# Kernel optimization log

Hardware: AMD Instinct MI355X
Metric: run time of the kernel (lower is better)

## Reference

```python
import jax, jax.numpy as jnp
import numpy as np

B, S, D, H = 2, 2048, 1024, 16
DK = D // H


def setup_inputs() -> dict:
    key = jax.random.key(0)
    ks = jax.random.split(key, 11)
    s = 1.0 / np.sqrt(D)
    return {
        "q": jax.random.normal(ks[0], (B, S, D), jnp.float32),
        "k": jax.random.normal(ks[1], (B, S, D), jnp.float32),
        "v": jax.random.normal(ks[2], (B, S, D), jnp.float32),
        "mask": jnp.ones((B, 1, S, S), jnp.int32),
        "Wq": jax.random.normal(ks[3], (D, D), jnp.float32) * s,
        "bq": jnp.zeros((D,), jnp.float32),
        "Wk": jax.random.normal(ks[4], (D, D), jnp.float32) * s,
        "bk": jnp.zeros((D,), jnp.float32),
        "Wv": jax.random.normal(ks[5], (D, D), jnp.float32) * s,
        "bv": jnp.zeros((D,), jnp.float32),
        "Wo": jax.random.normal(ks[6], (D, D), jnp.float32) * s,
        "bo": jnp.zeros((D,), jnp.float32),
    }


def reference(q, k, v, mask, Wq, bq, Wk, bk, Wv, bv, Wo, bo):
    # Note: original torch code calls non-in-place masked_fill and discards the
    # result, so the mask has no mathematical effect; we preserve that.
    qh = (q @ Wq + bq).reshape(B, S, H, DK).transpose(0, 2, 1, 3)  # [B,H,S,DK]
    kh = (k @ Wk + bk).reshape(B, S, H, DK).transpose(0, 2, 1, 3)
    vh = (v @ Wv + bv).reshape(B, S, H, DK).transpose(0, 2, 1, 3)
    scores = jnp.einsum("bhqd,bhkd->bhqk", qh, kh) / jnp.sqrt(jnp.float32(DK))
    attn = jax.nn.softmax(scores, axis=-1)
    out = jnp.einsum("bhqk,bhkd->bhqd", attn, vh)  # [B,H,S,DK]
    out = out.transpose(0, 2, 1, 3).reshape(B, S, D)
    return out @ Wo + bo
```

## Files before the change

### kernel.cpp

```cpp
#include <hip/hip_runtime.h>

#define S_LEN    2048
#define D_MODEL  1024
#define N_HEADS  16
#define HEAD_DIM 64
#define BATCH    2

typedef __bf16 bf16x8 __attribute__((ext_vector_type(8)));
typedef float  floatx4 __attribute__((ext_vector_type(4)));

__device__ __forceinline__ unsigned short f2bf(float f) {
    union { float f; unsigned int u; } v;
    v.f = f;
    unsigned int u = v.u;
    u += 0x7fffu + ((u >> 16) & 1u);
    return (unsigned short)(u >> 16);
}

__device__ __forceinline__ unsigned int pk_rne(float a, float b) {
    union { float f; unsigned int u; } ua, ub;
    ua.f = a; ub.f = b;
    unsigned int x = ua.u + 0x7fffu + ((ua.u >> 16) & 1u);
    unsigned int y = ub.u + 0x7fffu + ((ub.u >> 16) & 1u);
    return __builtin_amdgcn_perm(y, x, 0x07060302);
}

__device__ __forceinline__ void gload_lds16(const unsigned short* g, unsigned short* l) {
    __builtin_amdgcn_global_load_lds(
        (const __attribute__((address_space(1))) void*)(const void*)g,
        (__attribute__((address_space(3))) void*)(void*)l,
        16, 0, 0);
}

struct Conv3Args { const float* src[3]; unsigned short* dst[3]; };

__global__ void conv3_kernel(Conv3Args args, int n4) {
    int i = blockIdx.x * blockDim.x + threadIdx.x;
    const float* src = args.src[blockIdx.y];
    unsigned short* dst = args.dst[blockIdx.y];
    if (i < n4) {
        float4 f = reinterpret_cast<const float4*>(src)[i];
        ushort4 o;
        o.x = f2bf(f.x); o.y = f2bf(f.y); o.z = f2bf(f.z); o.w = f2bf(f.w);
        reinterpret_cast<ushort4*>(dst)[i] = o;
    }
}

struct Tr4Args { const float* W[4]; unsigned short* Wt[4]; };

__global__ void transpose4_kernel(Tr4Args args) {
    __shared__ unsigned short tile[64][65];
    const float* W = args.W[blockIdx.z];
    unsigned short* Wt = args.Wt[blockIdx.z];
    int n0 = blockIdx.x * 64, k0 = blockIdx.y * 64;
    for (int rep = 0; rep < 16; ++rep) {
        int e = rep * 256 + threadIdx.x;
        int kk = e >> 6, nn = e & 63;
        tile[kk][nn] = f2bf(W[(size_t)(k0 + kk) * D_MODEL + n0 + nn]);
    }
    __syncthreads();
    for (int rep = 0; rep < 16; ++rep) {
        int e = rep * 256 + threadIdx.x;
        int nn = e >> 6, kk = e & 63;
        Wt[(size_t)(n0 + nn) * D_MODEL + k0 + kk] = tile[kk][nn];
    }
}

template <int TM, int TN, int MODE>
__device__ __forceinline__
void gemm_body(const unsigned short* __restrict__ A,
               const unsigned short* __restrict__ Bt,
               const float* __restrict__ bias,
               void* __restrict__ out,
               int m0, int n0, float scale,
               unsigned short* As, unsigned short* Bs) {
    constexpr int MT = TM / 32;
    constexpr int NT = TN / 32;
    const int tid  = threadIdx.x;
    const int wid  = tid >> 6;
    const int lane = tid & 63;

    floatx4 acc[MT][NT];
#pragma unroll
    for (int i = 0; i < MT; ++i)
#pragma unroll
        for (int j = 0; j < NT; ++j) acc[i][j] = (floatx4)0.0f;

    const int srow = lane >> 2;
    const int gch  = (lane & 3) ^ ((srow >> 1) & 3);
    const int wr = (wid >> 1) * (TM / 2);
    const int wc = (wid & 1) * (TN / 2);
    const int fr = lane & 15;
    const int fq = lane >> 4;
    const int swz = (fq ^ ((fr >> 1) & 3)) * 8;

    for (int k0 = 0; k0 < D_MODEL; k0 += 32) {
        if (k0) __syncthreads();
#pragma unroll
        for (int ci = 0; ci < (TM + TN) / 64; ++ci) {
            const int c = wid + ci * 4;
            if (c < TM / 16) {
                const int row = c * 16 + srow;
                gload_lds16(A + (size_t)(m0 + row) * D_MODEL + k0 + gch * 8, As + c * 512);
            } else {
                const int cb = c - TM / 16;
                const int row = cb * 16 + srow;
                gload_lds16(Bt + (size_t)(n0 + row) * D_MODEL + k0 + gch * 8, Bs + cb * 512);
            }
        }
        __syncthreads();

        bf16x8 af[MT], bfv[NT];
#pragma unroll
        for (int t = 0; t < MT; ++t)
            af[t] = *reinterpret_cast<const bf16x8*>(As + (wr + t * 16 + fr) * 32 + swz);
#pragma unroll
        for (int t = 0; t < NT; ++t)
            bfv[t] = *reinterpret_cast<const bf16x8*>(Bs + (wc + t * 16 + fr) * 32 + swz);
#pragma unroll
        for (int mt = 0; mt < MT; ++mt)
#pragma unroll
            for (int nt = 0; nt < NT; ++nt)
                acc[mt][nt] = __builtin_amdgcn_mfma_f32_16x16x32_bf16(af[mt], bfv[nt], acc[mt][nt], 0, 0, 0);
    }

#pragma unroll
    for (int nt = 0; nt < NT; ++nt) {
        const int n = n0 + wc + nt * 16 + fr;
        const float bval = bias[n];
#pragma unroll
        for (int mt = 0; mt < MT; ++mt) {
#pragma unroll
            for (int r = 0; r < 4; ++r) {
                const int m = m0 + wr + mt * 16 + fq * 4 + r;
                const float val = (acc[mt][nt][r] + bval) * scale;
                if (MODE == 2) {
                    reinterpret_cast<float*>(out)[(size_t)m * D_MODEL + n] = val;
                } else {
                    const int b = m >> 11, s = m & (S_LEN - 1);
                    const int h = n >> 6, dk = n & 63;
                    const unsigned short o16 = f2bf(val);
                    if (MODE == 0)
                        reinterpret_cast<unsigned short*>(out)[(((size_t)(b * N_HEADS + h)) * S_LEN + s) * HEAD_DIM + dk] = o16;
                    else
                        reinterpret_cast<unsigned short*>(out)[(((size_t)(b * N_HEADS + h)) * HEAD_DIM + dk) * S_LEN + s] = o16;
                }
            }
        }
    }
}

struct QKVArgs {
    const unsigned short* A[3];
    const unsigned short* Bt[3];
    const float* bias[3];
    unsigned short* out[3];
};

__global__ __launch_bounds__(256)
void qkv_gemm_kernel(QKVArgs args) {
    __shared__ __align__(16) unsigned short As[128 * 32];
    __shared__ __align__(16) unsigned short Bs[128 * 32];
    const int z = blockIdx.z;
    const int m0 = blockIdx.y * 128;
    const int n0 = blockIdx.x * 128;
    if (z == 0)
        gemm_body<128, 128, 0>(args.A[0], args.Bt[0], args.bias[0], args.out[0], m0, n0, 0.18033688011112f, As, Bs);
    else if (z == 1)
        gemm_body<128, 128, 0>(args.A[1], args.Bt[1], args.bias[1], args.out[1], m0, n0, 1.0f, As, Bs);
    else
        gemm_body<128, 128, 1>(args.A[2], args.Bt[2], args.bias[2], args.out[2], m0, n0, 1.0f, As, Bs);
}

__global__ __launch_bounds__(256)
void oproj_gemm_kernel(const unsigned short* __restrict__ A,
                       const unsigned short* __restrict__ Bt,
                       const float* __restrict__ bias,
                       float* __restrict__ out) {
    __shared__ __align__(16) unsigned short As[64 * 32];
    __shared__ __align__(16) unsigned short Bs[128 * 32];
    gemm_body<64, 128, 2>(A, Bt, bias, out, blockIdx.y * 64, blockIdx.x * 128, 1.0f, As, Bs);
}

__global__ __launch_bounds__(256)
void attn_kernel(const unsigned short* __restrict__ qhp,
                 const unsigned short* __restrict__ khp,
                 const unsigned short* __restrict__ vtp,
                 unsigned short* __restrict__ outp) {
    __shared__ __align__(16) unsigned short Qs[128 * 64];
    __shared__ __align__(16) unsigned short Ks[64 * 64];
    __shared__ __align__(16) unsigned short Vs[64 * 64];
    __shared__ __align__(16) unsigned short Ps[4][32 * 72];

    const int tid  = threadIdx.x;
    const int wid  = tid >> 6;
    const int lane = tid & 63;
    const int b = blockIdx.z, h = blockIdx.y;
    const int q0 = blockIdx.x * 128;

    const unsigned short* qbase = qhp + (size_t)(b * N_HEADS + h) * S_LEN * HEAD_DIM;
    const unsigned short* kbase = khp + (size_t)(b * N_HEADS + h) * S_LEN * HEAD_DIM;
    const unsigned short* vbase = vtp + (size_t)(b * N_HEADS + h) * HEAD_DIM * S_LEN;

    const int srow = lane >> 3;
    const int gch  = (lane & 7) ^ srow;
    const int fr = lane & 15;
    const int fq = lane >> 4;
    const int sw7 = fr & 7;

#pragma unroll
    for (int i = 0; i < 4; ++i) {
        const int c = wid + i * 4;
        const int row = c * 8 + srow;
        gload_lds16(qbase + (size_t)(q0 + row) * HEAD_DIM + gch * 8, Qs + c * 512);
    }
    __syncthreads();

    bf16x8 qf[2][2];
#pragma unroll
    for (int qh2 = 0; qh2 < 2; ++qh2)
#pragma unroll
        for (int kk = 0; kk < 2; ++kk)
            qf[qh2][kk] = *reinterpret_cast<const bf16x8*>(
                Qs + (wid * 32 + qh2 * 16 + fr) * 64 + (((kk * 4 + fq) ^ sw7) * 8));

    floatx4 o_acc[2][4];
#pragma unroll
    for (int i = 0; i < 2; ++i)
#pragma unroll
        for (int j = 0; j < 4; ++j) o_acc[i][j] = (floatx4)0.0f;
    float l_sum[2] = {0.0f, 0.0f};

    for (int kv0 = 0; kv0 < S_LEN; kv0 += 64) {
        if (kv0) __syncthreads();
#pragma unroll
        for (int i = 0; i < 2; ++i) {
            const int c = wid + i * 4;
            const int row = c * 8 + srow;
            gload_lds16(kbase + (size_t)(kv0 + row) * HEAD_DIM + gch * 8, Ks + c * 512);
            gload_lds16(vbase + (size_t)row * S_LEN + kv0 + gch * 8,       Vs + c * 512);
        }
        __syncthreads();

        floatx4 st[2][4];
#pragma unroll
        for (int i = 0; i < 2; ++i)
#pragma unroll
            for (int j = 0; j < 4; ++j) st[i][j] = (floatx4)0.0f;
#pragma unroll
        for (int nt = 0; nt < 4; ++nt) {
#pragma unroll
            for (int kk = 0; kk < 2; ++kk) {
                bf16x8 kf = *reinterpret_cast<const bf16x8*>(
                    Ks + (nt * 16 + fr) * 64 + (((kk * 4 + fq) ^ sw7) * 8));
                st[0][nt] = __builtin_amdgcn_mfma_f32_16x16x32_bf16(kf, qf[0][kk], st[0][nt], 0, 0, 0);
                st[1][nt] = __builtin_amdgcn_mfma_f32_16x16x32_bf16(kf, qf[1][kk], st[1][nt], 0, 0, 0);
            }
        }

#pragma unroll
        for (int qh2 = 0; qh2 < 2; ++qh2) {
#pragma unroll
            for (int nt = 0; nt < 4; ++nt) {
                float p0 = __builtin_amdgcn_exp2f(st[qh2][nt][0]);
                float p1 = __builtin_amdgcn_exp2f(st[qh2][nt][1]);
                float p2 = __builtin_amdgcn_exp2f(st[qh2][nt][2]);
                float p3 = __builtin_amdgcn_exp2f(st[qh2][nt][3]);
                l_sum[qh2] += (p0 + p1) + (p2 + p3);
                uint2 w;
                w.x = pk_rne(p0, p1);
                w.y = pk_rne(p2, p3);
                *reinterpret_cast<uint2*>(Ps[wid] + (qh2 * 16 + fr) * 72 + nt * 16 + fq * 4) = w;
            }
        }
        __asm__ volatile("s_waitcnt lgkmcnt(0)" ::: "memory");

#pragma unroll
        for (int kk = 0; kk < 2; ++kk) {
            bf16x8 pf0 = *reinterpret_cast<const bf16x8*>(Ps[wid] + (fr)      * 72 + kk * 32 + fq * 8);
            bf16x8 pf1 = *reinterpret_cast<const bf16x8*>(Ps[wid] + (16 + fr) * 72 + kk * 32 + fq * 8);
#pragma unroll
            for (int dt = 0; dt < 4; ++dt) {
                bf16x8 vf = *reinterpret_cast<const bf16x8*>(
                    Vs + (dt * 16 + fr) * 64 + (((kk * 4 + fq) ^ sw7) * 8));
                o_acc[0][dt] = __builtin_amdgcn_mfma_f32_16x16x32_bf16(pf0, vf, o_acc[0][dt], 0, 0, 0);
                o_acc[1][dt] = __builtin_amdgcn_mfma_f32_16x16x32_bf16(pf1, vf, o_acc[1][dt], 0, 0, 0);
            }
        }
    }

#pragma unroll
    for (int qh2 = 0; qh2 < 2; ++qh2) {
        float l = l_sum[qh2];
        l += __shfl_xor(l, 16);
        l += __shfl_xor(l, 32);
        float linv[4];
#pragma unroll
        for (int r = 0; r < 4; ++r)
            linv[r] = __builtin_amdgcn_rcpf(__shfl(l, fq * 4 + r));
#pragma unroll
        for (int dt = 0; dt < 4; ++dt) {
#pragma unroll
            for (int r = 0; r < 4; ++r) {
                const int s  = q0 + wid * 32 + qh2 * 16 + fq * 4 + r;
                const int dk = dt * 16 + fr;
                const float val = o_acc[qh2][dt][r] * linv[r];
                outp[((size_t)(b * S_LEN + s)) * D_MODEL + h * HEAD_DIM + dk] = f2bf(val);
            }
        }
    }
}

extern "C" void kernel_launch(void* const* d_in, const int* in_sizes, int n_in,
                              void* d_out, int out_size, void* d_ws, size_t ws_size,
                              hipStream_t stream) {
    (void)in_sizes; (void)n_in; (void)out_size; (void)ws_size;
    const float* q  = (const float*)d_in[0];
    const float* k  = (const float*)d_in[1];
    const float* v  = (const float*)d_in[2];
    const float* Wq = (const float*)d_in[4];
    const float* bq = (const float*)d_in[5];
    const float* Wk = (const float*)d_in[6];
    const float* bk = (const float*)d_in[7];
    const float* Wv = (const float*)d_in[8];
    const float* bv = (const float*)d_in[9];
    const float* Wo = (const float*)d_in[10];
    const float* bo = (const float*)d_in[11];
    float* out = (float*)d_out;

    char* ws = (char*)d_ws;
    const size_t SZ_ACT = (size_t)BATCH * S_LEN * D_MODEL * 2;
    const size_t SZ_W   = (size_t)D_MODEL * D_MODEL * 2;
    unsigned short* qb   = (unsigned short*)(ws);
    unsigned short* kb   = (unsigned short*)(ws + SZ_ACT);
    unsigned short* vb   = (unsigned short*)(ws + 2 * SZ_ACT);
    unsigned short* Wqt  = (unsigned short*)(ws + 3 * SZ_ACT);
    unsigned short* Wkt  = (unsigned short*)(ws + 3 * SZ_ACT + SZ_W);
    unsigned short* Wvt  = (unsigned short*)(ws + 3 * SZ_ACT + 2 * SZ_W);
    unsigned short* Wot  = (unsigned short*)(ws + 3 * SZ_ACT + 3 * SZ_W);
    unsigned short* qhb  = (unsigned short*)(ws + 3 * SZ_ACT + 4 * SZ_W);
    unsigned short* khb  = (unsigned short*)(ws + 4 * SZ_ACT + 4 * SZ_W);
    unsigned short* vtb  = (unsigned short*)(ws + 5 * SZ_ACT + 4 * SZ_W);
    unsigned short* attn = qb;

    const int n4 = BATCH * S_LEN * D_MODEL / 4;

    Conv3Args cargs;
    cargs.src[0] = q;  cargs.src[1] = k;  cargs.src[2] = v;
    cargs.dst[0] = qb; cargs.dst[1] = kb; cargs.dst[2] = vb;
    conv3_kernel<<<dim3(n4 / 256, 3), 256, 0, stream>>>(cargs, n4);

    Tr4Args targs;
    targs.W[0] = Wq;  targs.W[1] = Wk;  targs.W[2] = Wv;  targs.W[3] = Wo;
    targs.Wt[0] = Wqt; targs.Wt[1] = Wkt; targs.Wt[2] = Wvt; targs.Wt[3] = Wot;
    transpose4_kernel<<<dim3(16, 16, 4), 256, 0, stream>>>(targs);

    QKVArgs gargs;
    gargs.A[0] = qb;  gargs.A[1] = kb;  gargs.A[2] = vb;
    gargs.Bt[0] = Wqt; gargs.Bt[1] = Wkt; gargs.Bt[2] = Wvt;
    gargs.bias[0] = bq; gargs.bias[1] = bk; gargs.bias[2] = bv;
    gargs.out[0] = qhb; gargs.out[1] = khb; gargs.out[2] = vtb;
    qkv_gemm_kernel<<<dim3(8, 32, 3), 256, 0, stream>>>(gargs);

    attn_kernel<<<dim3(S_LEN / 128, N_HEADS, BATCH), 256, 0, stream>>>(qhb, khb, vtb, attn);

    oproj_gemm_kernel<<<dim3(8, 64), 256, 0, stream>>>(attn, Wot, bo, out);
}
```

Baseline: 261.2 us.

## Merge conversion and transpose kernels; shrink attention blocks to 64 queries

Combines the fp32→bf16 activation conversion and the weight transpose into one prep kernel, saving a launch and letting the two jobs overlap. The attention kernel now uses 2 waves and 64 query rows per block instead of 4 waves and 128, doubling the grid to 1024 blocks for better occupancy and tail balance. Each block now loads K/V tiles for half as many queries, which doubles global K/V traffic per query, and each thread issues 4 load chunks instead of 2.

```diff
diff --git a/kernel.cpp b/kernel.cpp
--- a/kernel.cpp
+++ b/kernel.cpp
@@ -32,37 +32,42 @@
         16, 0, 0);
 }
 
-struct Conv3Args { const float* src[3]; unsigned short* dst[3]; };
-
-__global__ void conv3_kernel(Conv3Args args, int n4) {
-    int i = blockIdx.x * blockDim.x + threadIdx.x;
-    const float* src = args.src[blockIdx.y];
-    unsigned short* dst = args.dst[blockIdx.y];
-    if (i < n4) {
-        float4 f = reinterpret_cast<const float4*>(src)[i];
+struct PrepArgs {
+    const float* src[3]; unsigned short* dst[3];
+    const float* W[4];   unsigned short* Wt[4];
+};
+
+#define CONV_BLOCKS (3 * 4096)
+
+__global__ void prep_kernel(PrepArgs args) {
+    const int bid = blockIdx.x;
+    if (bid < CONV_BLOCKS) {
+        const int t   = bid >> 12;
+        const int blk = bid & 4095;
+        const int i   = blk * 256 + threadIdx.x;
+        float4 f = reinterpret_cast<const float4*>(args.src[t])[i];
         ushort4 o;
         o.x = f2bf(f.x); o.y = f2bf(f.y); o.z = f2bf(f.z); o.w = f2bf(f.w);
-        reinterpret_cast<ushort4*>(dst)[i] = o;
-    }
-}
-
-struct Tr4Args { const float* W[4]; unsigned short* Wt[4]; };
-
-__global__ void transpose4_kernel(Tr4Args args) {
-    __shared__ unsigned short tile[64][65];
-    const float* W = args.W[blockIdx.z];
-    unsigned short* Wt = args.Wt[blockIdx.z];
-    int n0 = blockIdx.x * 64, k0 = blockIdx.y * 64;
-    for (int rep = 0; rep < 16; ++rep) {
-        int e = rep * 256 + threadIdx.x;
-        int kk = e >> 6, nn = e & 63;
-        tile[kk][nn] = f2bf(W[(size_t)(k0 + kk) * D_MODEL + n0 + nn]);
-    }
-    __syncthreads();
-    for (int rep = 0; rep < 16; ++rep) {
-        int e = rep * 256 + threadIdx.x;
-        int nn = e >> 6, kk = e & 63;
-        Wt[(size_t)(n0 + nn) * D_MODEL + k0 + kk] = tile[kk][nn];
+        reinterpret_cast<ushort4*>(args.dst[t])[i] = o;
+    } else {
+        __shared__ unsigned short tile[64][65];
+        const int r  = bid - CONV_BLOCKS;
+        const int w  = r >> 8;
+        const int xy = r & 255;
+        const int n0 = (xy & 15) * 64, k0 = (xy >> 4) * 64;
+        const float* W = args.W[w];
+        unsigned short* Wt = args.Wt[w];
+        for (int rep = 0; rep < 16; ++rep) {
+            int e = rep * 256 + threadIdx.x;
+            int kk = e >> 6, nn = e & 63;
+            tile[kk][nn] = f2bf(W[(size_t)(k0 + kk) * D_MODEL + n0 + nn]);
+        }
+        __syncthreads();
+        for (int rep = 0; rep < 16; ++rep) {
+            int e = rep * 256 + threadIdx.x;
+            int nn = e >> 6, kk = e & 63;
+            Wt[(size_t)(n0 + nn) * D_MODEL + k0 + kk] = tile[kk][nn];
+        }
     }
 }
 
@@ -182,21 +187,21 @@
     gemm_body<64, 128, 2>(A, Bt, bias, out, blockIdx.y * 64, blockIdx.x * 128, 1.0f, As, Bs);
 }
 
-__global__ __launch_bounds__(256)
+__global__ __launch_bounds__(128)
 void attn_kernel(const unsigned short* __restrict__ qhp,
                  const unsigned short* __restrict__ khp,
                  const unsigned short* __restrict__ vtp,
                  unsigned short* __restrict__ outp) {
-    __shared__ __align__(16) unsigned short Qs[128 * 64];
+    __shared__ __align__(16) unsigned short Qs[64 * 64];
     __shared__ __align__(16) unsigned short Ks[64 * 64];
     __shared__ __align__(16) unsigned short Vs[64 * 64];
-    __shared__ __align__(16) unsigned short Ps[4][32 * 72];
+    __shared__ __align__(16) unsigned short Ps[2][32 * 72];
 
     const int tid  = threadIdx.x;
     const int wid  = tid >> 6;
     const int lane = tid & 63;
     const int b = blockIdx.z, h = blockIdx.y;
-    const int q0 = blockIdx.x * 128;
+    const int q0 = blockIdx.x * 64;
 
     const unsigned short* qbase = qhp + (size_t)(b * N_HEADS + h) * S_LEN * HEAD_DIM;
     const unsigned short* kbase = khp + (size_t)(b * N_HEADS + h) * S_LEN * HEAD_DIM;
@@ -210,7 +215,7 @@
 
 #pragma unroll
     for (int i = 0; i < 4; ++i) {
-        const int c = wid + i * 4;
+        const int c = wid * 4 + i;
         const int row = c * 8 + srow;
         gload_lds16(qbase + (size_t)(q0 + row) * HEAD_DIM + gch * 8, Qs + c * 512);
     }
@@ -234,8 +239,8 @@
     for (int kv0 = 0; kv0 < S_LEN; kv0 += 64) {
         if (kv0) __syncthreads();
 #pragma unroll
-        for (int i = 0; i < 2; ++i) {
-            const int c = wid + i * 4;
+        for (int i = 0; i < 4; ++i) {
+            const int c = wid * 4 + i;
             const int row = c * 8 + srow;
             gload_lds16(kbase + (size_t)(kv0 + row) * HEAD_DIM + gch * 8, Ks + c * 512);
             gload_lds16(vbase + (size_t)row * S_LEN + kv0 + gch * 8,       Vs + c * 512);
@@ -343,17 +348,12 @@
     unsigned short* vtb  = (unsigned short*)(ws + 5 * SZ_ACT + 4 * SZ_W);
     unsigned short* attn = qb;
 
-    const int n4 = BATCH * S_LEN * D_MODEL / 4;
-
-    Conv3Args cargs;
-    cargs.src[0] = q;  cargs.src[1] = k;  cargs.src[2] = v;
-    cargs.dst[0] = qb; cargs.dst[1] = kb; cargs.dst[2] = vb;
-    conv3_kernel<<<dim3(n4 / 256, 3), 256, 0, stream>>>(cargs, n4);
-
-    Tr4Args targs;
-    targs.W[0] = Wq;  targs.W[1] = Wk;  targs.W[2] = Wv;  targs.W[3] = Wo;
-    targs.Wt[0] = Wqt; targs.Wt[1] = Wkt; targs.Wt[2] = Wvt; targs.Wt[3] = Wot;
-    transpose4_kernel<<<dim3(16, 16, 4), 256, 0, stream>>>(targs);
+    PrepArgs pargs;
+    pargs.src[0] = q;  pargs.src[1] = k;  pargs.src[2] = v;
+    pargs.dst[0] = qb; pargs.dst[1] = kb; pargs.dst[2] = vb;
+    pargs.W[0] = Wq;  pargs.W[1] = Wk;  pargs.W[2] = Wv;  pargs.W[3] = Wo;
+    pargs.Wt[0] = Wqt; pargs.Wt[1] = Wkt; pargs.Wt[2] = Wvt; pargs.Wt[3] = Wot;
+    prep_kernel<<<dim3(CONV_BLOCKS + 1024), 256, 0, stream>>>(pargs);
 
     QKVArgs gargs;
     gargs.A[0] = qb;  gargs.A[1] = kb;  gargs.A[2] = vb;
@@ -362,7 +362,7 @@
     gargs.out[0] = qhb; gargs.out[1] = khb; gargs.out[2] = vtb;
     qkv_gemm_kernel<<<dim3(8, 32, 3), 256, 0, stream>>>(gargs);
 
-    attn_kernel<<<dim3(S_LEN / 128, N_HEADS, BATCH), 256, 0, stream>>>(qhb, khb, vtb, attn);
+    attn_kernel<<<dim3(S_LEN / 64, N_HEADS, BATCH), 128, 0, stream>>>(qhb, khb, vtb, attn);
 
     oproj_gemm_kernel<<<dim3(8, 64), 256, 0, stream>>>(attn, Wot, bo, out);
 }
```

Measured after the change: 259.0 us. About the same (-0.8%).
